# Optimization experiments

Hardware: AMD Instinct MI355X
Metric: run time of the kernel (lower is better)

The kernel has to match this reference:

```python
import jax, jax.numpy as jnp
import numpy as np

B, T, D, H = 2, 2048, 1024, 16
HD = D // H  # head_dim = 64


def setup_inputs() -> dict:
    key = jax.random.key(0)
    ks = jax.random.split(key, 9)
    s = 0.02
    return {
        "hidden_states": jax.random.normal(ks[0], (B, T, D), jnp.float32),
        "attention_mask": jnp.zeros((B, 1, T, T), jnp.float32),
        "Wq": jax.random.normal(ks[1], (D, D), jnp.float32) * s,
        "bq": jax.random.normal(ks[2], (D,), jnp.float32) * s,
        "Wk": jax.random.normal(ks[3], (D, D), jnp.float32) * s,
        "bk": jax.random.normal(ks[4], (D,), jnp.float32) * s,
        "Wv": jax.random.normal(ks[5], (D, D), jnp.float32) * s,
        "bv": jax.random.normal(ks[6], (D,), jnp.float32) * s,
        "Wo": jax.random.normal(ks[7], (D, D), jnp.float32) * s,
        "bo": jax.random.normal(ks[8], (D,), jnp.float32) * s,
    }


def _heads(x):
    # [B, T, D] -> [B, H, T, HD]
    return x.reshape(B, -1, H, HD).transpose(0, 2, 1, 3)


def reference(hidden_states, attention_mask, Wq, bq, Wk, bk, Wv, bv, Wo, bo):
    scaling = HD ** -0.5
    # nn.Linear: x @ W.T + b; query scaled BEFORE head split (as in source)
    q = _heads((hidden_states @ Wq.T + bq) * scaling)  # [B,H,T,HD]
    k = _heads(hidden_states @ Wk.T + bk)
    v = _heads(hidden_states @ Wv.T + bv)
    # eager QK^T -> +mask -> softmax -> @V (full [B,H,T,T] materialized)
    attn = jnp.einsum('bhqd,bhkd->bhqk', q, k) + attention_mask
    attn = jax.nn.softmax(attn, axis=-1)
    out = jnp.einsum('bhqk,bhkd->bhqd', attn, v)  # [B,H,T,HD]
    out = out.transpose(0, 2, 1, 3).reshape(B, -1, D)
    return out @ Wo.T + bo
```

## Files before the change

### kernel.cpp

```cpp
#include <hip/hip_runtime.h>
#include <hip/hip_bf16.h>

typedef __bf16 v8bf __attribute__((ext_vector_type(8)));
typedef unsigned short v8us __attribute__((ext_vector_type(8)));
typedef float v4f __attribute__((ext_vector_type(4)));

#define B_ 2
#define T_ 2048
#define D_ 1024
#define H_ 16
#define HD_ 64
#define M_ 4096
#define LDST 88
#define PSTR 72
#define LOG2E 1.44269504f

static __device__ __forceinline__ unsigned short f2bfbits(float f) {
    __hip_bfloat16 h = __float2bfloat16(f);
    unsigned short u;
    __builtin_memcpy(&u, &h, 2);
    return u;
}

static __device__ __forceinline__ v8us load8_f32_to_bf16(const float* g) {
    float4 fa = *(const float4*)g;
    float4 fb = *(const float4*)(g + 4);
    v8us p;
    p[0] = f2bfbits(fa.x); p[1] = f2bfbits(fa.y);
    p[2] = f2bfbits(fa.z); p[3] = f2bfbits(fa.w);
    p[4] = f2bfbits(fb.x); p[5] = f2bfbits(fb.y);
    p[6] = f2bfbits(fb.z); p[7] = f2bfbits(fb.w);
    return p;
}

static __device__ __forceinline__ void async16(const void* g, void* l) {
    __builtin_amdgcn_global_load_lds(
        (const __attribute__((address_space(1))) void*)g,
        (__attribute__((address_space(3))) void*)l, 16, 0, 0);
}

__global__ __launch_bounds__(256) void cvt_multi(
    const float* __restrict__ hs, const float* __restrict__ wq,
    const float* __restrict__ wk, const float* __restrict__ wv,
    const float* __restrict__ wo, __hip_bfloat16* __restrict__ hsb,
    __hip_bfloat16* __restrict__ wqb, __hip_bfloat16* __restrict__ wkb,
    __hip_bfloat16* __restrict__ wvb, __hip_bfloat16* __restrict__ wob) {
    int bid = blockIdx.x;
    const float* src;
    __hip_bfloat16* dst;
    int off;
    if (bid < 2048) {
        src = hs; dst = hsb; off = bid;
    } else {
        int w = (bid - 2048) >> 9;
        off = (bid - 2048) & 511;
        src = (w == 0) ? wq : (w == 1) ? wk : (w == 2) ? wv : wo;
        dst = (w == 0) ? wqb : (w == 1) ? wkb : (w == 2) ? wvb : wob;
    }
    int i = (off * 256 + threadIdx.x) * 8;
    *(v8us*)&dst[i] = load8_f32_to_bf16(&src[i]);
}

__global__ __launch_bounds__(256) void gemm_qkv(
    const __hip_bfloat16* __restrict__ A, const __hip_bfloat16* __restrict__ W,
    const float* __restrict__ bq_, const float* __restrict__ bk_,
    const float* __restrict__ bv_, __hip_bfloat16* __restrict__ qo,
    __hip_bfloat16* __restrict__ ko, __hip_bfloat16* __restrict__ vo) {
    __shared__ __hip_bfloat16 sA[128 * 64];
    __shared__ __hip_bfloat16 sW[128 * 64];
    const int tid = threadIdx.x;
    const int wid = tid >> 6, lane = tid & 63;
    const int quad = lane >> 4, lq = lane & 15;
    const int wm = wid & 1, wn = wid >> 1;
    const int n0 = blockIdx.x * 128, m0 = blockIdx.y * 128;
    const int mid = n0 >> 10;
    const float* bias = (mid == 0) ? bq_ : (mid == 1) ? bk_ : bv_;

    v4f acc[4][4] = {};

    for (int k0 = 0; k0 < 1024; k0 += 64) {
        __syncthreads();
        for (int it = 0; it < 8; ++it) {
            int Lc = it * 256 + tid;
            int l1 = Lc & 1023;
            int row = l1 >> 3, pos = l1 & 7;
            if (it < 4)
                async16(&A[(size_t)(m0 + row) * 1024 + k0 + ((pos ^ (row & 7)) * 8)],
                        &sA[l1 * 8]);
            else
                async16(&W[(size_t)(n0 + row) * 1024 + k0 + ((pos ^ (row & 7)) * 8)],
                        &sW[l1 * 8]);
        }
        __syncthreads();
        for (int c = 0; c < 2; ++c) {
            v8bf af[4], wf[4];
            for (int mf = 0; mf < 4; ++mf) {
                int row = wm * 64 + mf * 16 + lq;
                af[mf] = *(const v8bf*)&sA[row * 64 + (((c * 4 + quad) ^ (lq & 7)) * 8)];
            }
            for (int nf = 0; nf < 4; ++nf) {
                int row = wn * 64 + nf * 16 + lq;
                wf[nf] = *(const v8bf*)&sW[row * 64 + (((c * 4 + quad) ^ (lq & 7)) * 8)];
            }
            for (int mf = 0; mf < 4; ++mf)
                for (int nf = 0; nf < 4; ++nf)
                    acc[mf][nf] = __builtin_amdgcn_mfma_f32_16x16x32_bf16(
                        af[mf], wf[nf], acc[mf][nf], 0, 0, 0);
        }
    }

    for (int nf = 0; nf < 4; ++nf) {
        int n = n0 + wn * 64 + nf * 16 + lq;
        int nl = n & 1023;
        int hh = nl >> 6, dd = nl & 63;
        float bvv = bias[nl];
        for (int mf = 0; mf < 4; ++mf) {
            int mbase = m0 + wm * 64 + mf * 16 + quad * 4;
            int bb = mbase >> 11;
            if (mid == 2) {
                int t0 = mbase & 2047;
                ushort4 pk;
                pk.x = f2bfbits(acc[mf][nf][0] + bvv);
                pk.y = f2bfbits(acc[mf][nf][1] + bvv);
                pk.z = f2bfbits(acc[mf][nf][2] + bvv);
                pk.w = f2bfbits(acc[mf][nf][3] + bvv);
                *(ushort4*)&vo[(((size_t)(bb * H_ + hh)) * HD_ + dd) * T_ + t0] = pk;
            } else {
                __hip_bfloat16* dst = (mid == 0) ? qo : ko;
                float sc = (mid == 0) ? 0.125f * LOG2E : 1.0f;
                for (int r = 0; r < 4; ++r) {
                    int m = mbase + r;
                    int t = m & 2047;
                    dst[(((size_t)(bb * H_ + hh)) * T_ + t) * HD_ + dd] =
                        __float2bfloat16((acc[mf][nf][r] + bvv) * sc);
                }
            }
        }
    }
}

__global__ __launch_bounds__(256) void gemm_out(
    const __hip_bfloat16* __restrict__ A, const __hip_bfloat16* __restrict__ W,
    const float* __restrict__ bias, float* __restrict__ out) {
    __shared__ __hip_bfloat16 sA[128 * 64];
    __shared__ __hip_bfloat16 sW[64 * 64];
    const int tid = threadIdx.x;
    const int wid = tid >> 6, lane = tid & 63;
    const int quad = lane >> 4, lq = lane & 15;
    const int wm = wid & 1, wn = wid >> 1;
    const int n0 = blockIdx.x * 64, m0 = blockIdx.y * 128;

    v4f acc[4][2] = {};

    for (int k0 = 0; k0 < 1024; k0 += 64) {
        __syncthreads();
        for (int it = 0; it < 4; ++it) {
            int Lc = wid * 256 + it * 64 + lane;
            int row = Lc >> 3, pos = Lc & 7;
            async16(&A[(size_t)(m0 + row) * 1024 + k0 + ((pos ^ (row & 7)) * 8)],
                    &sA[Lc * 8]);
        }
        for (int it = 0; it < 2; ++it) {
            int Lc = wid * 128 + it * 64 + lane;
            int row = Lc >> 3, pos = Lc & 7;
            async16(&W[(size_t)(n0 + row) * 1024 + k0 + ((pos ^ (row & 7)) * 8)],
                    &sW[Lc * 8]);
        }
        __syncthreads();
        for (int c = 0; c < 2; ++c) {
            v8bf af[4], wf[2];
            for (int mf = 0; mf < 4; ++mf) {
                int row = wm * 64 + mf * 16 + lq;
                af[mf] = *(const v8bf*)&sA[row * 64 + (((c * 4 + quad) ^ (lq & 7)) * 8)];
            }
            for (int nf = 0; nf < 2; ++nf) {
                int row = wn * 32 + nf * 16 + lq;
                wf[nf] = *(const v8bf*)&sW[row * 64 + (((c * 4 + quad) ^ (lq & 7)) * 8)];
            }
            for (int mf = 0; mf < 4; ++mf)
                for (int nf = 0; nf < 2; ++nf)
                    acc[mf][nf] = __builtin_amdgcn_mfma_f32_16x16x32_bf16(
                        af[mf], wf[nf], acc[mf][nf], 0, 0, 0);
        }
    }
    for (int nf = 0; nf < 2; ++nf) {
        int n = n0 + wn * 32 + nf * 16 + lq;
        float bv = bias[n];
        for (int mf = 0; mf < 4; ++mf) {
            int mbase = m0 + wm * 64 + mf * 16 + quad * 4;
            for (int r = 0; r < 4; ++r)
                out[(size_t)(mbase + r) * 1024 + n] = acc[mf][nf][r] + bv;
        }
    }
}

template <int EPI, bool ABF16, bool WBF16>
__global__ __launch_bounds__(256) void gemm128(
    const void* __restrict__ Av, const void* __restrict__ Wv_,
    const float* __restrict__ bias, void* __restrict__ outv) {
    __shared__ __hip_bfloat16 sA[128 * LDST];
    __shared__ __hip_bfloat16 sW[128 * LDST];
    const int tid = threadIdx.x;
    const int wid = tid >> 6, lane = tid & 63;
    const int quad = lane >> 4, lq = lane & 15;
    const int wm = wid & 1, wn = wid >> 1;
    const int n0 = blockIdx.x * 128, m0 = blockIdx.y * 128;
    v4f acc[4][4] = {};
    for (int k0 = 0; k0 < 1024; k0 += 64) {
        __syncthreads();
        for (int i = 0; i < 4; ++i) {
            int f = i * 256 + tid;
            int row = f >> 3, ch = f & 7;
            if constexpr (ABF16) {
                const __hip_bfloat16* A = (const __hip_bfloat16*)Av;
                *(int4*)&sA[row * LDST + ch * 8] =
                    *(const int4*)&A[(size_t)(m0 + row) * 1024 + k0 + ch * 8];
            } else {
                const float* A = (const float*)Av;
                *(v8us*)&sA[row * LDST + ch * 8] =
                    load8_f32_to_bf16(&A[(size_t)(m0 + row) * 1024 + k0 + ch * 8]);
            }
            if constexpr (WBF16) {
                const __hip_bfloat16* W = (const __hip_bfloat16*)Wv_;
                *(int4*)&sW[row * LDST + ch * 8] =
                    *(const int4*)&W[(size_t)(n0 + row) * 1024 + k0 + ch * 8];
            } else {
                const float* W = (const float*)Wv_;
                *(v8us*)&sW[row * LDST + ch * 8] =
                    load8_f32_to_bf16(&W[(size_t)(n0 + row) * 1024 + k0 + ch * 8]);
            }
        }
        __syncthreads();
        for (int c = 0; c < 2; ++c) {
            v8bf af[4], wf[4];
            for (int mf = 0; mf < 4; ++mf)
                af[mf] = *(const v8bf*)&sA[(wm * 64 + mf * 16 + lq) * LDST + c * 32 + quad * 8];
            for (int nf = 0; nf < 4; ++nf)
                wf[nf] = *(const v8bf*)&sW[(wn * 64 + nf * 16 + lq) * LDST + c * 32 + quad * 8];
            for (int mf = 0; mf < 4; ++mf)
                for (int nf = 0; nf < 4; ++nf)
                    acc[mf][nf] = __builtin_amdgcn_mfma_f32_16x16x32_bf16(
                        af[mf], wf[nf], acc[mf][nf], 0, 0, 0);
        }
    }
    for (int nf = 0; nf < 4; ++nf) {
        int n = n0 + wn * 64 + nf * 16 + lq;
        float bv = bias[n];
        for (int mf = 0; mf < 4; ++mf) {
            int mbase = m0 + wm * 64 + mf * 16 + quad * 4;
            if constexpr (EPI == 2) {
                __hip_bfloat16* out = (__hip_bfloat16*)outv;
                int bb = mbase >> 11, t0 = mbase & 2047;
                int hh = n >> 6, dd = n & 63;
                ushort4 pk;
                pk.x = f2bfbits(acc[mf][nf][0] + bv);
                pk.y = f2bfbits(acc[mf][nf][1] + bv);
                pk.z = f2bfbits(acc[mf][nf][2] + bv);
                pk.w = f2bfbits(acc[mf][nf][3] + bv);
                *(ushort4*)&out[(((size_t)(bb * H_ + hh)) * HD_ + dd) * T_ + t0] = pk;
            } else {
                for (int r = 0; r < 4; ++r) {
                    int m = mbase + r;
                    float v = acc[mf][nf][r] + bv;
                    if constexpr (EPI == 0) {
                        __hip_bfloat16* out = (__hip_bfloat16*)outv;
                        v *= 0.125f * LOG2E;
                        int bb = m >> 11, t = m & 2047, hh = n >> 6, dd = n & 63;
                        out[(((size_t)(bb * H_ + hh)) * T_ + t) * HD_ + dd] = __float2bfloat16(v);
                    } else if constexpr (EPI == 1) {
                        __hip_bfloat16* out = (__hip_bfloat16*)outv;
                        int bb = m >> 11, t = m & 2047, hh = n >> 6, dd = n & 63;
                        out[(((size_t)(bb * H_ + hh)) * T_ + t) * HD_ + dd] = __float2bfloat16(v);
                    } else {
                        float* out = (float*)outv;
                        out[(size_t)m * 1024 + n] = v;
                    }
                }
            }
        }
    }
}

__global__ __launch_bounds__(256) void attn_kernel(
    const __hip_bfloat16* __restrict__ q, const __hip_bfloat16* __restrict__ k,
    const __hip_bfloat16* __restrict__ vt, const float* __restrict__ mask,
    __hip_bfloat16* __restrict__ out) {
    __shared__ __hip_bfloat16 sK[128 * 64];
    __shared__ __hip_bfloat16 sV[64 * 128];
    __shared__ __hip_bfloat16 pT[4][32 * PSTR];
    const int tid = threadIdx.x;
    const int wid = tid >> 6, lane = tid & 63;
    const int quad = lane >> 4, lq = lane & 15;
    const int bh = blockIdx.y;
    const int b = bh >> 4, h = bh & 15;
    const int qb = blockIdx.x * 128 + wid * 32;
    const int qt0 = qb + lq, qt1 = qt0 + 16;

    v8bf bq0[2], bq1[2];
    for (int c = 0; c < 2; ++c) {
        bq0[c] = *(const v8bf*)&q[((size_t)bh * T_ + qt0) * HD_ + c * 32 + quad * 8];
        bq1[c] = *(const v8bf*)&q[((size_t)bh * T_ + qt1) * HD_ + c * 32 + quad * 8];
    }
    const float* mrow0 = mask + ((size_t)b * T_ + qt0) * T_;
    const float* mrow1 = mask + ((size_t)b * T_ + qt1) * T_;
    const __hip_bfloat16* kbase = k + (size_t)bh * T_ * HD_;
    const __hip_bfloat16* vbase = vt + (size_t)bh * HD_ * T_;

    float l0 = 0.f, l1 = 0.f;
    v4f o0[4] = {}, o1[4] = {};

    for (int kt0 = 0; kt0 < T_; kt0 += 128) {
        float4 ma0[4], ma1[4];
        for (int ki = 0; ki < 4; ++ki) {
            ma0[ki] = *(const float4*)&mrow0[kt0 + ki * 16 + quad * 4];
            ma1[ki] = *(const float4*)&mrow1[kt0 + ki * 16 + quad * 4];
        }
        __syncthreads();
        for (int it = 0; it < 4; ++it) {
            int Lc = it * 256 + tid;
            int row = Lc >> 3, pos = Lc & 7;
            async16(&kbase[(size_t)(kt0 + row) * HD_ + ((pos ^ (row & 7)) * 8)],
                    &sK[Lc * 8]);
        }
        for (int it = 0; it < 4; ++it) {
            int Lc = it * 256 + tid;
            int row = Lc >> 4, pos = Lc & 15;
            async16(&vbase[(size_t)row * T_ + kt0 + ((pos ^ (row & 15)) * 8)],
                    &sV[Lc * 8]);
        }
        __syncthreads();

        float4 mb0[4], mb1[4];
        for (int ki = 0; ki < 4; ++ki) {
            mb0[ki] = *(const float4*)&mrow0[kt0 + 64 + ki * 16 + quad * 4];
            mb1[ki] = *(const float4*)&mrow1[kt0 + 64 + ki * 16 + quad * 4];
        }

        for (int hf = 0; hf < 2; ++hf) {
            const int ko = hf * 64;
            float4* mg0 = hf ? mb0 : ma0;
            float4* mg1 = hf ? mb1 : ma1;
            v4f st0[4] = {}, st1[4] = {};
            for (int ki = 0; ki < 4; ++ki)
                for (int c = 0; c < 2; ++c) {
                    int row = ko + ki * 16 + lq;
                    v8bf ka = *(const v8bf*)&sK[row * 64 + (((c * 4 + quad) ^ (row & 7)) * 8)];
                    st0[ki] = __builtin_amdgcn_mfma_f32_16x16x32_bf16(ka, bq0[c], st0[ki], 0, 0, 0);
                    st1[ki] = __builtin_amdgcn_mfma_f32_16x16x32_bf16(ka, bq1[c], st1[ki], 0, 0, 0);
                }
            for (int ki = 0; ki < 4; ++ki)
                for (int r = 0; r < 4; ++r) {
                    st0[ki][r] = exp2f(fmaf((&mg0[ki].x)[r], LOG2E, st0[ki][r]));
                    st1[ki][r] = exp2f(fmaf((&mg1[ki].x)[r], LOG2E, st1[ki][r]));
                    l0 += st0[ki][r];
                    l1 += st1[ki][r];
                }
            for (int ki = 0; ki < 4; ++ki) {
                ushort4 p0, p1;
                p0.x = f2bfbits(st0[ki][0]); p0.y = f2bfbits(st0[ki][1]);
                p0.z = f2bfbits(st0[ki][2]); p0.w = f2bfbits(st0[ki][3]);
                p1.x = f2bfbits(st1[ki][0]); p1.y = f2bfbits(st1[ki][1]);
                p1.z = f2bfbits(st1[ki][2]); p1.w = f2bfbits(st1[ki][3]);
                *(ushort4*)&pT[wid][lq * PSTR + ki * 16 + quad * 4] = p0;
                *(ushort4*)&pT[wid][(16 + lq) * PSTR + ki * 16 + quad * 4] = p1;
            }
            for (int c = 0; c < 2; ++c) {
                v8bf pb0 = *(const v8bf*)&pT[wid][lq * PSTR + c * 32 + quad * 8];
                v8bf pb1 = *(const v8bf*)&pT[wid][(16 + lq) * PSTR + c * 32 + quad * 8];
                for (int nt = 0; nt < 4; ++nt) {
                    int row = nt * 16 + lq;
                    int cs = hf * 8 + c * 4 + quad;
                    v8bf va = *(const v8bf*)&sV[row * 128 + ((cs ^ (row & 15)) * 8)];
                    o0[nt] = __builtin_amdgcn_mfma_f32_16x16x32_bf16(va, pb0, o0[nt], 0, 0, 0);
                    o1[nt] = __builtin_amdgcn_mfma_f32_16x16x32_bf16(va, pb1, o1[nt], 0, 0, 0);
                }
            }
        }
    }

    l0 += __shfl_xor(l0, 16); l0 += __shfl_xor(l0, 32);
    l1 += __shfl_xor(l1, 16); l1 += __shfl_xor(l1, 32);
    float i0 = 1.0f / l0, i1 = 1.0f / l1;
    for (int nt = 0; nt < 4; ++nt) {
        ushort4 p0, p1;
        p0.x = f2bfbits(o0[nt][0] * i0); p0.y = f2bfbits(o0[nt][1] * i0);
        p0.z = f2bfbits(o0[nt][2] * i0); p0.w = f2bfbits(o0[nt][3] * i0);
        p1.x = f2bfbits(o1[nt][0] * i1); p1.y = f2bfbits(o1[nt][1] * i1);
        p1.z = f2bfbits(o1[nt][2] * i1); p1.w = f2bfbits(o1[nt][3] * i1);
        *(ushort4*)&out[((size_t)b * T_ + qt0) * D_ + h * HD_ + nt * 16 + quad * 4] = p0;
        *(ushort4*)&out[((size_t)b * T_ + qt1) * D_ + h * HD_ + nt * 16 + quad * 4] = p1;
    }
}

extern "C" void kernel_launch(void* const* d_in, const int* in_sizes, int n_in,
                              void* d_out, int out_size, void* d_ws, size_t ws_size,
                              hipStream_t stream) {
    const float* hs   = (const float*)d_in[0];
    const float* mask = (const float*)d_in[1];
    const float* Wq   = (const float*)d_in[2];
    const float* bq   = (const float*)d_in[3];
    const float* Wk   = (const float*)d_in[4];
    const float* bk   = (const float*)d_in[5];
    const float* Wv   = (const float*)d_in[6];
    const float* bv   = (const float*)d_in[7];
    const float* Wo   = (const float*)d_in[8];
    const float* bo   = (const float*)d_in[9];
    float* out = (float*)d_out;

    const size_t TEN = (size_t)B_ * H_ * T_ * HD_;
    const size_t WEL = (size_t)D_ * D_;
    __hip_bfloat16* q_ws  = (__hip_bfloat16*)d_ws;
    __hip_bfloat16* k_ws  = q_ws + TEN;
    __hip_bfloat16* vt_ws = k_ws + TEN;
    __hip_bfloat16* at_ws = vt_ws + TEN;

    dim3 qkvgrid(3072 / 128, M_ / 128);
    dim3 outgrid(D_ / 64, M_ / 128);
    dim3 ogrid(D_ / 128, M_ / 128);
    dim3 agrid(T_ / 128, B_ * H_);

    const size_t need = (4 * TEN + TEN + 4 * WEL) * sizeof(__hip_bfloat16);
    if (ws_size >= need) {
        __hip_bfloat16* hsb = at_ws + TEN;
        __hip_bfloat16* wqb = hsb + TEN;
        __hip_bfloat16* wkb = wqb + WEL;
        __hip_bfloat16* wvb = wkb + WEL;
        __hip_bfloat16* wob = wvb + WEL;
        cvt_multi<<<2048 + 4 * 512, 256, 0, stream>>>(hs, Wq, Wk, Wv, Wo,
                                                      hsb, wqb, wkb, wvb, wob);
        gemm_qkv<<<qkvgrid, 256, 0, stream>>>(hsb, wqb, bq, bk, bv, q_ws, k_ws, vt_ws);
        attn_kernel<<<agrid, 256, 0, stream>>>(q_ws, k_ws, vt_ws, mask, at_ws);
        gemm_out<<<outgrid, 256, 0, stream>>>(at_ws, wob, bo, out);
    } else {
        gemm128<0, false, false><<<ogrid, 256, 0, stream>>>(hs, Wq, bq, q_ws);
        gemm128<1, false, false><<<ogrid, 256, 0, stream>>>(hs, Wk, bk, k_ws);
        gemm128<2, false, false><<<ogrid, 256, 0, stream>>>(hs, Wv, bv, vt_ws);
        attn_kernel<<<agrid, 256, 0, stream>>>(q_ws, k_ws, vt_ws, mask, at_ws);
        gemm128<3, true, false><<<ogrid, 256, 0, stream>>>(at_ws, Wo, bo, out);
    }
}
```

Measured before the change: 262.5 us.

## Double-buffer K/V tiles in attention and prefetch the next tile during compute

The attention loop moves from 128-key tiles with a load-then-compute pattern and two barriers per step to 64-key tiles in two shared-memory buffers. The loads for the next tile are issued right after a single barrier, so global-to-LDS traffic overlaps the MFMA and softmax work on the current tile. The V layout and the swizzle are adapted to the 64-wide tiles, and exp2f is replaced with the hardware exp2 builtin. In exchange the loop runs twice as many iterations, and the mask loads are no longer issued ahead of the barrier.

Result: slower. 270.8 us (+3.2%).

```diff
diff --git a/kernel.cpp b/kernel.cpp
--- a/kernel.cpp
+++ b/kernel.cpp
@@ -285,8 +285,8 @@
     const __hip_bfloat16* __restrict__ q, const __hip_bfloat16* __restrict__ k,
     const __hip_bfloat16* __restrict__ vt, const float* __restrict__ mask,
     __hip_bfloat16* __restrict__ out) {
-    __shared__ __hip_bfloat16 sK[128 * 64];
-    __shared__ __hip_bfloat16 sV[64 * 128];
+    __shared__ __hip_bfloat16 sK[2][64 * 64];
+    __shared__ __hip_bfloat16 sV[2][64 * 64];
     __shared__ __hip_bfloat16 pT[4][32 * PSTR];
     const int tid = threadIdx.x;
     const int wid = tid >> 6, lane = tid & 63;
@@ -306,74 +306,69 @@
     const __hip_bfloat16* kbase = k + (size_t)bh * T_ * HD_;
     const __hip_bfloat16* vbase = vt + (size_t)bh * HD_ * T_;
 
+    auto stage = [&](int kt0, int buf) {
+        for (int it2 = 0; it2 < 2; ++it2) {
+            int Lc = wid * 128 + it2 * 64 + lane;
+            int row = Lc >> 3, pos = Lc & 7;
+            async16(&kbase[(size_t)(kt0 + row) * HD_ + ((pos ^ (row & 7)) * 8)],
+                    &sK[buf][Lc * 8]);
+        }
+        for (int it2 = 0; it2 < 2; ++it2) {
+            int Lc = wid * 128 + it2 * 64 + lane;
+            int row = Lc >> 3, pos = Lc & 7;
+            async16(&vbase[(size_t)row * T_ + kt0 + ((pos ^ (row & 7)) * 8)],
+                    &sV[buf][Lc * 8]);
+        }
+    };
+
     float l0 = 0.f, l1 = 0.f;
     v4f o0[4] = {}, o1[4] = {};
 
-    for (int kt0 = 0; kt0 < T_; kt0 += 128) {
-        float4 ma0[4], ma1[4];
+    stage(0, 0);
+
+    for (int itn = 0; itn < T_ / 64; ++itn) {
+        const int kt0 = itn * 64, buf = itn & 1;
+        __syncthreads();
+        if (itn + 1 < T_ / 64) stage(kt0 + 64, buf ^ 1);
+
+        float4 mg0[4], mg1[4];
         for (int ki = 0; ki < 4; ++ki) {
-            ma0[ki] = *(const float4*)&mrow0[kt0 + ki * 16 + quad * 4];
-            ma1[ki] = *(const float4*)&mrow1[kt0 + ki * 16 + quad * 4];
-        }
-        __syncthreads();
-        for (int it = 0; it < 4; ++it) {
-            int Lc = it * 256 + tid;
-            int row = Lc >> 3, pos = Lc & 7;
-            async16(&kbase[(size_t)(kt0 + row) * HD_ + ((pos ^ (row & 7)) * 8)],
-                    &sK[Lc * 8]);
-        }
-        for (int it = 0; it < 4; ++it) {
-            int Lc = it * 256 + tid;
-            int row = Lc >> 4, pos = Lc & 15;
-            async16(&vbase[(size_t)row * T_ + kt0 + ((pos ^ (row & 15)) * 8)],
-                    &sV[Lc * 8]);
-        }
-        __syncthreads();
-
-        float4 mb0[4], mb1[4];
+            mg0[ki] = *(const float4*)&mrow0[kt0 + ki * 16 + quad * 4];
+            mg1[ki] = *(const float4*)&mrow1[kt0 + ki * 16 + quad * 4];
+        }
+
+        v4f st0[4] = {}, st1[4] = {};
+        for (int ki = 0; ki < 4; ++ki)
+            for (int c = 0; c < 2; ++c) {
+                int row = ki * 16 + lq;
+                v8bf ka = *(const v8bf*)&sK[buf][row * 64 + (((c * 4 + quad) ^ (lq & 7)) * 8)];
+                st0[ki] = __builtin_amdgcn_mfma_f32_16x16x32_bf16(ka, bq0[c], st0[ki], 0, 0, 0);
+                st1[ki] = __builtin_amdgcn_mfma_f32_16x16x32_bf16(ka, bq1[c], st1[ki], 0, 0, 0);
+            }
+        for (int ki = 0; ki < 4; ++ki)
+            for (int r = 0; r < 4; ++r) {
+                st0[ki][r] = __builtin_amdgcn_exp2f(fmaf((&mg0[ki].x)[r], LOG2E, st0[ki][r]));
+                st1[ki][r] = __builtin_amdgcn_exp2f(fmaf((&mg1[ki].x)[r], LOG2E, st1[ki][r]));
+                l0 += st0[ki][r];
+                l1 += st1[ki][r];
+            }
         for (int ki = 0; ki < 4; ++ki) {
-            mb0[ki] = *(const float4*)&mrow0[kt0 + 64 + ki * 16 + quad * 4];
-            mb1[ki] = *(const float4*)&mrow1[kt0 + 64 + ki * 16 + quad * 4];
-        }
-
-        for (int hf = 0; hf < 2; ++hf) {
-            const int ko = hf * 64;
-            float4* mg0 = hf ? mb0 : ma0;
-            float4* mg1 = hf ? mb1 : ma1;
-            v4f st0[4] = {}, st1[4] = {};
-            for (int ki = 0; ki < 4; ++ki)
-                for (int c = 0; c < 2; ++c) {
-                    int row = ko + ki * 16 + lq;
-                    v8bf ka = *(const v8bf*)&sK[row * 64 + (((c * 4 + quad) ^ (row & 7)) * 8)];
-                    st0[ki] = __builtin_amdgcn_mfma_f32_16x16x32_bf16(ka, bq0[c], st0[ki], 0, 0, 0);
-                    st1[ki] = __builtin_amdgcn_mfma_f32_16x16x32_bf16(ka, bq1[c], st1[ki], 0, 0, 0);
-                }
-            for (int ki = 0; ki < 4; ++ki)
-                for (int r = 0; r < 4; ++r) {
-                    st0[ki][r] = exp2f(fmaf((&mg0[ki].x)[r], LOG2E, st0[ki][r]));
-                    st1[ki][r] = exp2f(fmaf((&mg1[ki].x)[r], LOG2E, st1[ki][r]));
-                    l0 += st0[ki][r];
-                    l1 += st1[ki][r];
-                }
-            for (int ki = 0; ki < 4; ++ki) {
-                ushort4 p0, p1;
-                p0.x = f2bfbits(st0[ki][0]); p0.y = f2bfbits(st0[ki][1]);
-                p0.z = f2bfbits(st0[ki][2]); p0.w = f2bfbits(st0[ki][3]);
-                p1.x = f2bfbits(st1[ki][0]); p1.y = f2bfbits(st1[ki][1]);
-                p1.z = f2bfbits(st1[ki][2]); p1.w = f2bfbits(st1[ki][3]);
-                *(ushort4*)&pT[wid][lq * PSTR + ki * 16 + quad * 4] = p0;
-                *(ushort4*)&pT[wid][(16 + lq) * PSTR + ki * 16 + quad * 4] = p1;
-            }
-            for (int c = 0; c < 2; ++c) {
-                v8bf pb0 = *(const v8bf*)&pT[wid][lq * PSTR + c * 32 + quad * 8];
-                v8bf pb1 = *(const v8bf*)&pT[wid][(16 + lq) * PSTR + c * 32 + quad * 8];
-                for (int nt = 0; nt < 4; ++nt) {
-                    int row = nt * 16 + lq;
-                    int cs = hf * 8 + c * 4 + quad;
-                    v8bf va = *(const v8bf*)&sV[row * 128 + ((cs ^ (row & 15)) * 8)];
-                    o0[nt] = __builtin_amdgcn_mfma_f32_16x16x32_bf16(va, pb0, o0[nt], 0, 0, 0);
-                    o1[nt] = __builtin_amdgcn_mfma_f32_16x16x32_bf16(va, pb1, o1[nt], 0, 0, 0);
-                }
+            ushort4 p0, p1;
+            p0.x = f2bfbits(st0[ki][0]); p0.y = f2bfbits(st0[ki][1]);
+            p0.z = f2bfbits(st0[ki][2]); p0.w = f2bfbits(st0[ki][3]);
+            p1.x = f2bfbits(st1[ki][0]); p1.y = f2bfbits(st1[ki][1]);
+            p1.z = f2bfbits(st1[ki][2]); p1.w = f2bfbits(st1[ki][3]);
+            *(ushort4*)&pT[wid][lq * PSTR + ki * 16 + quad * 4] = p0;
+            *(ushort4*)&pT[wid][(16 + lq) * PSTR + ki * 16 + quad * 4] = p1;
+        }
+        for (int c = 0; c < 2; ++c) {
+            v8bf pb0 = *(const v8bf*)&pT[wid][lq * PSTR + c * 32 + quad * 8];
+            v8bf pb1 = *(const v8bf*)&pT[wid][(16 + lq) * PSTR + c * 32 + quad * 8];
+            for (int nt = 0; nt < 4; ++nt) {
+                int row = nt * 16 + lq;
+                v8bf va = *(const v8bf*)&sV[buf][row * 64 + (((c * 4 + quad) ^ (lq & 7)) * 8)];
+                o0[nt] = __builtin_amdgcn_mfma_f32_16x16x32_bf16(va, pb0, o0[nt], 0, 0, 0);
+                o1[nt] = __builtin_amdgcn_mfma_f32_16x16x32_bf16(va, pb1, o1[nt], 0, 0, 0);
             }
         }
     }
```
